# Performance work log

Hardware: AMD Instinct MI355X
Metric: run time of the kernel (lower is better)

The kernel has to match this reference:

```python
import jax, jax.numpy as jnp
import numpy as np

S, C, HF, WF = 6, 64, 44, 80          # cameras, feat channels, feat H, feat W
H_IMG, W_IMG = 352.0, 640.0           # full image size (opt.height/opt.width)
Z, Y, X = 16, 100, 100                # voxel grid (opt.voxels_size)
XMIN, XMAX = -40.0, 40.0
YMIN, YMAX = -40.0, 40.0
ZMIN, ZMAX = -1.0, 5.4
EPS = 1e-6


def setup_inputs() -> dict:
    key = jax.random.key(0)
    features = jax.random.normal(jax.random.fold_in(key, 0), (S, C, HF, WF), dtype=jnp.float32)
    # intrinsics at full image resolution
    K = np.eye(4, dtype=np.float32)
    K[0, 0] = 500.0; K[1, 1] = 500.0
    K[0, 2] = W_IMG / 2.0; K[1, 2] = H_IMG / 2.0
    pix_T_cams = np.tile(K[None], (S, 1, 1))
    # 6-camera surround rig: cam0_T_camX rigid transforms (columns = camera axes in ref frame)
    mats = []
    for i in range(S):
        th = 2.0 * np.pi * i / S
        c, s = np.cos(th), np.sin(th)
        T = np.eye(4, dtype=np.float32)
        T[:3, 0] = [-s, c, 0.0]          # camera x (right)
        T[:3, 1] = [0.0, 0.0, -1.0]      # camera y (down)
        T[:3, 2] = [c, s, 0.0]           # camera z (forward)
        T[:3, 3] = [0.5 * c, 0.5 * s, 1.5]
        mats.append(T)
    cam0_T_camXs = np.stack(mats).astype(np.float32)
    return {"features": features,
            "pix_T_cams": jnp.asarray(pix_T_cams),
            "cam0_T_camXs": jnp.asarray(cam0_T_camXs)}


def _safe_inverse(T):
    # rigid 4x4 inverse: [R t] -> [R^T, -R^T t]
    R = T[:, :3, :3]
    t = T[:, :3, 3]
    Rt = jnp.swapaxes(R, 1, 2)
    tt = -jnp.einsum('sij,sj->si', Rt, t)
    inv = jnp.zeros_like(T)
    inv = inv.at[:, :3, :3].set(Rt).at[:, :3, 3].set(tt).at[:, 3, 3].set(1.0)
    return inv


def _voxel_centers():
    # ref-frame coordinates of voxel centers, flattened [Z*Y*X, 3] with x fastest
    vx = (XMAX - XMIN) / X
    vy = (YMAX - YMIN) / Y
    vz = (ZMAX - ZMIN) / Z
    xs = XMIN + vx * (jnp.arange(X, dtype=jnp.float32) + 0.5)
    ys = YMIN + vy * (jnp.arange(Y, dtype=jnp.float32) + 0.5)
    zs = ZMIN + vz * (jnp.arange(Z, dtype=jnp.float32) + 0.5)
    zz, yy, xx = jnp.meshgrid(zs, ys, xs, indexing='ij')
    return jnp.stack([xx, yy, zz], axis=-1).reshape(-1, 3)


def _bilinear(img, x, y):
    # img: [C,H,W]; x,y: [N] pixel coords; zero padding outside
    Hh, Ww = img.shape[-2], img.shape[-1]
    x0 = jnp.floor(x)
    y0 = jnp.floor(y)
    wx1 = x - x0
    wy1 = y - y0

    def corner(xi, yi, w):
        valid = (xi >= 0) & (xi < Ww) & (yi >= 0) & (yi < Hh)
        xc = jnp.clip(xi, 0, Ww - 1).astype(jnp.int32)
        yc = jnp.clip(yi, 0, Hh - 1).astype(jnp.int32)
        return img[:, yc, xc] * (w * valid)[None, :]

    return (corner(x0, y0, (1 - wx1) * (1 - wy1))
            + corner(x0 + 1, y0, wx1 * (1 - wy1))
            + corner(x0, y0 + 1, (1 - wx1) * wy1)
            + corner(x0 + 1, y0 + 1, wx1 * wy1))  # [C,N]


def reference(features, pix_T_cams, cam0_T_camXs):
    camXs_T_cam0 = _safe_inverse(cam0_T_camXs)
    sx, sy = WF / W_IMG, HF / H_IMG
    scale = jnp.diag(jnp.array([sx, sy, 1.0, 1.0], jnp.float32))
    featpix_T_cams = jnp.einsum('ij,sjk->sik', scale, pix_T_cams)
    pix_T_cam0 = jnp.einsum('sij,sjk->sik', featpix_T_cams, camXs_T_cam0)

    xyz0 = _voxel_centers()                                  # [N,3]
    xyz1 = jnp.concatenate([xyz0, jnp.ones((xyz0.shape[0], 1), jnp.float32)], -1)
    xyz_pix = jnp.einsum('sij,nj->sni', pix_T_cam0, xyz1)    # [S,N,4]
    z_cam = jnp.einsum('sj,nj->sn', camXs_T_cam0[:, 2, :], xyz1)  # camX-frame depth

    denom = jnp.maximum(xyz_pix[..., 2], 1e-6)
    x_pix = xyz_pix[..., 0] / denom
    y_pix = xyz_pix[..., 1] / denom
    valid = ((x_pix > -0.5) & (x_pix < WF - 0.5)
             & (y_pix > -0.5) & (y_pix < HF - 0.5)
             & (z_cam > 0.0))

    # grid_sample(align_corners=False) with norm 2*(p/W)-1 samples at pixel p-0.5
    samp = jax.vmap(_bilinear)(features, x_pix - 0.5, y_pix - 0.5)  # [S,C,N]
    feat_mems = samp * valid[:, None, :].astype(samp.dtype)
    feat_mems = feat_mems.reshape(S, C, Z, Y, X)[None]              # [1,S,C,Z,Y,X]

    mask = (jnp.abs(feat_mems) > 0).astype(feat_mems.dtype)
    feat_mem = (feat_mems * mask).sum(1) / (mask.sum(1) + EPS)      # masked mean over cams
    return jnp.transpose(feat_mem, (0, 1, 4, 3, 2))                 # [1,C,X,Y,Z]
```

## Files before the change

### kernel.cpp

```cpp
#include <hip/hip_runtime.h>

#define NS 6
#define NC 64
#define HF 44
#define WF 80
#define HW (HF * WF)
#define NZ 16
#define NY 100
#define NX 100
#define XYZ (NX * NY * NZ)
#define COLS 4
#define NPAR (COLS * NZ * NS)

typedef float v4f __attribute__((ext_vector_type(4)));

__device__ void compute_mats(int s, const float* __restrict__ pix,
                             const float* __restrict__ c0TX,
                             float* __restrict__ mats) {
    const float* T = c0TX + s * 16;
    float inv[4][4];
    for (int i = 0; i < 3; ++i) {
        for (int j = 0; j < 3; ++j) inv[i][j] = T[j * 4 + i];
        inv[i][3] = -(T[0 * 4 + i] * T[0 * 4 + 3] +
                      T[1 * 4 + i] * T[1 * 4 + 3] +
                      T[2 * 4 + i] * T[2 * 4 + 3]);
    }
    inv[3][0] = 0.f; inv[3][1] = 0.f; inv[3][2] = 0.f; inv[3][3] = 1.f;
    const float sx = (float)WF / 640.0f;
    const float sy = (float)HF / 352.0f;
    const float* K = pix + s * 16;
    float fp[3][4];
    for (int j = 0; j < 4; ++j) {
        fp[0][j] = sx * K[0 * 4 + j];
        fp[1][j] = sy * K[1 * 4 + j];
        fp[2][j] = K[2 * 4 + j];
    }
    float* M = mats + s * 16;
    for (int i = 0; i < 3; ++i)
        for (int j = 0; j < 4; ++j) {
            float acc = 0.f;
            for (int k = 0; k < 4; ++k) acc += fp[i][k] * inv[k][j];
            M[i * 4 + j] = acc;
        }
    for (int j = 0; j < 4; ++j) M[12 + j] = inv[2][j];
}

__global__ __launch_bounds__(256) void transpose_feat(
        const float* __restrict__ in, float* __restrict__ outT,
        const float* __restrict__ pix, const float* __restrict__ c0TX,
        float* __restrict__ mats) {
    __shared__ float tile[64 * 65];
    int b = blockIdx.x;
    int t = threadIdx.x;
    if (b == 0 && t < NS) compute_mats(t, pix, c0TX, mats);
    int s = b / 55;
    int hw0 = (b % 55) * 64;
#pragma unroll
    for (int i = 0; i < 4; ++i) {
        int e = t + i * 256;
        int c = e >> 4, wg = e & 15;
        float4 f = *(const float4*)(in + ((size_t)(s * NC + c)) * HW + hw0 + wg * 4);
        tile[c * 65 + wg * 4 + 0] = f.x;
        tile[c * 65 + wg * 4 + 1] = f.y;
        tile[c * 65 + wg * 4 + 2] = f.z;
        tile[c * 65 + wg * 4 + 3] = f.w;
    }
    __syncthreads();
#pragma unroll
    for (int i = 0; i < 4; ++i) {
        int e = t + i * 256;
        int hwl = e >> 4, cg = e & 15;
        float4 f;
        f.x = tile[(cg * 4 + 0) * 65 + hwl];
        f.y = tile[(cg * 4 + 1) * 65 + hwl];
        f.z = tile[(cg * 4 + 2) * 65 + hwl];
        f.w = tile[(cg * 4 + 3) * 65 + hwl];
        *(float4*)(outT + ((size_t)s * HW + hw0 + hwl) * NC + cg * 4) = f;
    }
}

__global__ void setup_mats(const float* __restrict__ pix,
                           const float* __restrict__ c0TX,
                           float* __restrict__ mats) {
    int s = threadIdx.x;
    if (s < NS) compute_mats(s, pix, c0TX, mats);
}

template <bool TRANS>
__global__ __launch_bounds__(256) void volpool(
        const float* __restrict__ feat,
        const float* __restrict__ mats,
        float* __restrict__ out) {
    __shared__ float4 wts[NPAR];
    __shared__ int4   offs[NPAR];
    __shared__ int    vflags[NPAR];
    __shared__ int    vidx[COLS][NZ][NS];
    __shared__ int    nvalid[COLS][NZ];
    __shared__ float  ostage[COLS][NC * 17];

    int t = threadIdx.x;
    int b = blockIdx.x;
    int x0 = (b % (NX / COLS)) * COLS;
    int y  = b / (NX / COLS);

    for (int p = t; p < NPAR; p += 256) {
        int col  = p / 96;
        int rest = p - col * 96;
        int s = rest % NS;
        int z = rest / NS;
        const float* M = mats + s * 16;
        float xw = -40.0f + 0.8f * ((float)(x0 + col) + 0.5f);
        float yw = -40.0f + 0.8f * ((float)y + 0.5f);
        float zw = -1.0f + 0.4f * ((float)z + 0.5f);
        float px = M[0] * xw + M[1] * yw + M[2]  * zw + M[3];
        float py = M[4] * xw + M[5] * yw + M[6]  * zw + M[7];
        float pz = M[8] * xw + M[9] * yw + M[10] * zw + M[11];
        float zc = M[12] * xw + M[13] * yw + M[14] * zw + M[15];
        float denom = fmaxf(pz, 1e-6f);
        float xp = px / denom, yp = py / denom;
        bool valid = (xp > -0.5f) & (xp < (float)WF - 0.5f) &
                     (yp > -0.5f) & (yp < (float)HF - 0.5f) & (zc > 0.0f);
        vflags[p] = valid ? 1 : 0;
        if (valid) {
            float xs = xp - 0.5f, ys = yp - 0.5f;
            float x0f = floorf(xs), y0f = floorf(ys);
            float wx1 = xs - x0f, wy1 = ys - y0f;
            float wx0 = 1.f - wx1, wy0 = 1.f - wy1;
            int xi0 = (int)x0f, yi0 = (int)y0f;
            int xi1 = xi0 + 1, yi1 = yi0 + 1;
            bool bx0 = (xi0 >= 0) & (xi0 < WF);
            bool bx1 = (xi1 >= 0) & (xi1 < WF);
            bool by0 = (yi0 >= 0) & (yi0 < HF);
            bool by1 = (yi1 >= 0) & (yi1 < HF);
            int x0c = min(max(xi0, 0), WF - 1);
            int x1c = min(max(xi1, 0), WF - 1);
            int y0c = min(max(yi0, 0), HF - 1);
            int y1c = min(max(yi1, 0), HF - 1);
            float4 w;
            w.x = wx0 * wy0 * (float)(bx0 & by0);
            w.y = wx1 * wy0 * (float)(bx1 & by0);
            w.z = wx0 * wy1 * (float)(bx0 & by1);
            w.w = wx1 * wy1 * (float)(bx1 & by1);
            int p00 = y0c * WF + x0c, p10 = y0c * WF + x1c;
            int p01 = y1c * WF + x0c, p11 = y1c * WF + x1c;
            int4 o;
            if (TRANS) {
                o.x = (s * HW + p00) * NC;
                o.y = (s * HW + p10) * NC;
                o.z = (s * HW + p01) * NC;
                o.w = (s * HW + p11) * NC;
            } else {
                o.x = s * NC * HW + p00;
                o.y = s * NC * HW + p10;
                o.z = s * NC * HW + p01;
                o.w = s * NC * HW + p11;
            }
            wts[p] = w;
            offs[p] = o;
        }
    }
    __syncthreads();

    if (t < COLS * NZ) {
        int col = t >> 4, z = t & 15;
        int base = col * 96 + z * NS;
        int n = 0;
        for (int s = 0; s < NS; ++s)
            if (vflags[base + s]) vidx[col][z][n++] = base + s;
        nvalid[col][z] = n;
    }
    __syncthreads();

    int cg = t & 15, z = t >> 4;
    int ch4 = cg << 2;
#pragma unroll
    for (int col = 0; col < COLS; ++col) {
        float4 sum = make_float4(0.f, 0.f, 0.f, 0.f);
        float4 cnt = make_float4(0.f, 0.f, 0.f, 0.f);
        int nv = nvalid[col][z];
        for (int j = 0; j < nv; ++j) {
            int idx = vidx[col][z][j];
            float4 w = wts[idx];
            int4 o = offs[idx];
            float4 f00, f10, f01, f11;
            if (TRANS) {
                f00 = *(const float4*)(feat + o.x + ch4);
                f10 = *(const float4*)(feat + o.y + ch4);
                f01 = *(const float4*)(feat + o.z + ch4);
                f11 = *(const float4*)(feat + o.w + ch4);
            } else {
                f00.x = feat[o.x + (ch4 + 0) * HW]; f00.y = feat[o.x + (ch4 + 1) * HW];
                f00.z = feat[o.x + (ch4 + 2) * HW]; f00.w = feat[o.x + (ch4 + 3) * HW];
                f10.x = feat[o.y + (ch4 + 0) * HW]; f10.y = feat[o.y + (ch4 + 1) * HW];
                f10.z = feat[o.y + (ch4 + 2) * HW]; f10.w = feat[o.y + (ch4 + 3) * HW];
                f01.x = feat[o.z + (ch4 + 0) * HW]; f01.y = feat[o.z + (ch4 + 1) * HW];
                f01.z = feat[o.z + (ch4 + 2) * HW]; f01.w = feat[o.z + (ch4 + 3) * HW];
                f11.x = feat[o.w + (ch4 + 0) * HW]; f11.y = feat[o.w + (ch4 + 1) * HW];
                f11.z = feat[o.w + (ch4 + 2) * HW]; f11.w = feat[o.w + (ch4 + 3) * HW];
            }
            float vx = w.x * f00.x + w.y * f10.x + w.z * f01.x + w.w * f11.x;
            float vy = w.x * f00.y + w.y * f10.y + w.z * f01.y + w.w * f11.y;
            float vz = w.x * f00.z + w.y * f10.z + w.z * f01.z + w.w * f11.z;
            float vw = w.x * f00.w + w.y * f10.w + w.z * f01.w + w.w * f11.w;
            sum.x += vx; cnt.x += (vx != 0.0f) ? 1.0f : 0.0f;
            sum.y += vy; cnt.y += (vy != 0.0f) ? 1.0f : 0.0f;
            sum.z += vz; cnt.z += (vz != 0.0f) ? 1.0f : 0.0f;
            sum.w += vw; cnt.w += (vw != 0.0f) ? 1.0f : 0.0f;
        }
        float* os = &ostage[col][0];
        os[(ch4 + 0) * 17 + z] = sum.x / (cnt.x + 1e-6f);
        os[(ch4 + 1) * 17 + z] = sum.y / (cnt.y + 1e-6f);
        os[(ch4 + 2) * 17 + z] = sum.z / (cnt.z + 1e-6f);
        os[(ch4 + 3) * 17 + z] = sum.w / (cnt.w + 1e-6f);
    }
    __syncthreads();

    int c = t >> 2, zq = t & 3;
#pragma unroll
    for (int col = 0; col < COLS; ++col) {
        v4f v4;
        v4.x = ostage[col][c * 17 + zq * 4 + 0];
        v4.y = ostage[col][c * 17 + zq * 4 + 1];
        v4.z = ostage[col][c * 17 + zq * 4 + 2];
        v4.w = ostage[col][c * 17 + zq * 4 + 3];
        float* o = out + (size_t)c * XYZ +
                   ((size_t)(x0 + col) * NY + y) * NZ + zq * 4;
        __builtin_nontemporal_store(v4, (v4f*)o);
    }
}

extern "C" void kernel_launch(void* const* d_in, const int* in_sizes, int n_in,
                              void* d_out, int out_size, void* d_ws, size_t ws_size,
                              hipStream_t stream) {
    const float* features = (const float*)d_in[0];
    const float* pix      = (const float*)d_in[1];
    const float* c0TX     = (const float*)d_in[2];
    float* out   = (float*)d_out;
    float* mats  = (float*)d_ws;
    float* featT = (float*)((char*)d_ws + 512);
    size_t need = 512 + sizeof(float) * (size_t)NS * HW * NC;

    if (ws_size >= need) {
        hipLaunchKernelGGL(transpose_feat, dim3(NS * 55), dim3(256), 0, stream,
                           features, featT, pix, c0TX, mats);
        hipLaunchKernelGGL((volpool<true>), dim3((NX / COLS) * NY), dim3(256),
                           0, stream, featT, mats, out);
    } else {
        hipLaunchKernelGGL(setup_mats, dim3(1), dim3(64), 0, stream,
                           pix, c0TX, mats);
        hipLaunchKernelGGL((volpool<false>), dim3((NX / COLS) * NY), dim3(256),
                           0, stream, features, mats, out);
    }
}
```

Measured before the change: 89.16 us.

## Process one voxel column per block with compacted samples and software-pipelined gathers

Each block now handles a single (x,y) column instead of four, so the grid has four times as many smaller blocks. Valid camera samples' weights and offsets are compacted into per-z arrays, so the hot loop no longer reads through an index table. The gather loop is software-pipelined so the next camera's loads are issued before the current sample is accumulated. Offsets are precomputed as byte offsets, and the divide by count is replaced by a small reciprocal lookup table. The trade-off is more blocks and more per-block setup and sync overhead, with fewer independent loads in flight per thread.

```diff
diff --git a/kernel.cpp b/kernel.cpp
--- a/kernel.cpp
+++ b/kernel.cpp
@@ -9,8 +9,6 @@
 #define NY 100
 #define NX 100
 #define XYZ (NX * NY * NZ)
-#define COLS 4
-#define NPAR (COLS * NZ * NS)
 
 typedef float v4f __attribute__((ext_vector_type(4)));
 
@@ -91,25 +89,23 @@
         const float* __restrict__ feat,
         const float* __restrict__ mats,
         float* __restrict__ out) {
-    __shared__ float4 wts[NPAR];
-    __shared__ int4   offs[NPAR];
-    __shared__ int    vflags[NPAR];
-    __shared__ int    vidx[COLS][NZ][NS];
-    __shared__ int    nvalid[COLS][NZ];
-    __shared__ float  ostage[COLS][NC * 17];
+    __shared__ float4 wts_raw[96];
+    __shared__ int4   offs_raw[96];
+    __shared__ int    vflags[96];
+    __shared__ float4 wts_c[NZ][NS];
+    __shared__ int4   offs_c[NZ][NS];
+    __shared__ int    nvalid[NZ];
+    __shared__ float  rlut[8];
+    __shared__ float  ostage[NC * 17];
 
     int t = threadIdx.x;
     int b = blockIdx.x;
-    int x0 = (b % (NX / COLS)) * COLS;
-    int y  = b / (NX / COLS);
-
-    for (int p = t; p < NPAR; p += 256) {
-        int col  = p / 96;
-        int rest = p - col * 96;
-        int s = rest % NS;
-        int z = rest / NS;
+    int x = b % NX, y = b / NX;
+
+    if (t < 96) {
+        int s = t % NS, z = t / NS;
         const float* M = mats + s * 16;
-        float xw = -40.0f + 0.8f * ((float)(x0 + col) + 0.5f);
+        float xw = -40.0f + 0.8f * ((float)x + 0.5f);
         float yw = -40.0f + 0.8f * ((float)y + 0.5f);
         float zw = -1.0f + 0.4f * ((float)z + 0.5f);
         float px = M[0] * xw + M[1] * yw + M[2]  * zw + M[3];
@@ -120,7 +116,7 @@
         float xp = px / denom, yp = py / denom;
         bool valid = (xp > -0.5f) & (xp < (float)WF - 0.5f) &
                      (yp > -0.5f) & (yp < (float)HF - 0.5f) & (zc > 0.0f);
-        vflags[p] = valid ? 1 : 0;
+        vflags[t] = valid ? 1 : 0;
         if (valid) {
             float xs = xp - 0.5f, ys = yp - 0.5f;
             float x0f = floorf(xs), y0f = floorf(ys);
@@ -145,88 +141,121 @@
             int p01 = y1c * WF + x0c, p11 = y1c * WF + x1c;
             int4 o;
             if (TRANS) {
-                o.x = (s * HW + p00) * NC;
-                o.y = (s * HW + p10) * NC;
-                o.z = (s * HW + p01) * NC;
-                o.w = (s * HW + p11) * NC;
+                o.x = (s * HW + p00) << 8;
+                o.y = (s * HW + p10) << 8;
+                o.z = (s * HW + p01) << 8;
+                o.w = (s * HW + p11) << 8;
             } else {
-                o.x = s * NC * HW + p00;
-                o.y = s * NC * HW + p10;
-                o.z = s * NC * HW + p01;
-                o.w = s * NC * HW + p11;
+                o.x = (s * NC * HW + p00) << 2;
+                o.y = (s * NC * HW + p10) << 2;
+                o.z = (s * NC * HW + p01) << 2;
+                o.w = (s * NC * HW + p11) << 2;
             }
-            wts[p] = w;
-            offs[p] = o;
-        }
-    }
-    __syncthreads();
-
-    if (t < COLS * NZ) {
-        int col = t >> 4, z = t & 15;
-        int base = col * 96 + z * NS;
+            wts_raw[t] = w;
+            offs_raw[t] = o;
+        }
+    }
+    if (t >= 96 && t < 104) {
+        int k = t - 96;
+        rlut[k] = 1.0f / ((float)k + 1e-6f);
+    }
+    __syncthreads();
+
+    if (t < NZ) {
+        int base = t * NS;
         int n = 0;
-        for (int s = 0; s < NS; ++s)
-            if (vflags[base + s]) vidx[col][z][n++] = base + s;
-        nvalid[col][z] = n;
+        for (int s = 0; s < NS; ++s) {
+            if (vflags[base + s]) {
+                wts_c[t][n] = wts_raw[base + s];
+                offs_c[t][n] = offs_raw[base + s];
+                ++n;
+            }
+        }
+        nvalid[t] = n;
     }
     __syncthreads();
 
     int cg = t & 15, z = t >> 4;
     int ch4 = cg << 2;
-#pragma unroll
-    for (int col = 0; col < COLS; ++col) {
-        float4 sum = make_float4(0.f, 0.f, 0.f, 0.f);
-        float4 cnt = make_float4(0.f, 0.f, 0.f, 0.f);
-        int nv = nvalid[col][z];
-        for (int j = 0; j < nv; ++j) {
-            int idx = vidx[col][z][j];
-            float4 w = wts[idx];
-            int4 o = offs[idx];
-            float4 f00, f10, f01, f11;
+    const char* fb = (const char*)feat + (TRANS ? (cg << 4) : 0);
+    float4 sum = make_float4(0.f, 0.f, 0.f, 0.f);
+    int cx = 0, cy = 0, cz = 0, cw = 0;
+    int nv = nvalid[z];
+    if (nv > 0) {
+        float4 w = wts_c[z][0];
+        int4 o = offs_c[z][0];
+        float4 f00, f10, f01, f11;
+        if (TRANS) {
+            f00 = *(const float4*)(fb + o.x);
+            f10 = *(const float4*)(fb + o.y);
+            f01 = *(const float4*)(fb + o.z);
+            f11 = *(const float4*)(fb + o.w);
+        } else {
+            const float* fp = (const float*)fb;
+            int e00 = o.x >> 2, e10 = o.y >> 2, e01 = o.z >> 2, e11 = o.w >> 2;
+            f00.x = fp[e00 + (ch4+0)*HW]; f00.y = fp[e00 + (ch4+1)*HW];
+            f00.z = fp[e00 + (ch4+2)*HW]; f00.w = fp[e00 + (ch4+3)*HW];
+            f10.x = fp[e10 + (ch4+0)*HW]; f10.y = fp[e10 + (ch4+1)*HW];
+            f10.z = fp[e10 + (ch4+2)*HW]; f10.w = fp[e10 + (ch4+3)*HW];
+            f01.x = fp[e01 + (ch4+0)*HW]; f01.y = fp[e01 + (ch4+1)*HW];
+            f01.z = fp[e01 + (ch4+2)*HW]; f01.w = fp[e01 + (ch4+3)*HW];
+            f11.x = fp[e11 + (ch4+0)*HW]; f11.y = fp[e11 + (ch4+1)*HW];
+            f11.z = fp[e11 + (ch4+2)*HW]; f11.w = fp[e11 + (ch4+3)*HW];
+        }
+        for (int j = 1; j < nv; ++j) {
+            float4 w2 = wts_c[z][j];
+            int4 o2 = offs_c[z][j];
+            float4 g00, g10, g01, g11;
             if (TRANS) {
-                f00 = *(const float4*)(feat + o.x + ch4);
-                f10 = *(const float4*)(feat + o.y + ch4);
-                f01 = *(const float4*)(feat + o.z + ch4);
-                f11 = *(const float4*)(feat + o.w + ch4);
+                g00 = *(const float4*)(fb + o2.x);
+                g10 = *(const float4*)(fb + o2.y);
+                g01 = *(const float4*)(fb + o2.z);
+                g11 = *(const float4*)(fb + o2.w);
             } else {
-                f00.x = feat[o.x + (ch4 + 0) * HW]; f00.y = feat[o.x + (ch4 + 1) * HW];
-                f00.z = feat[o.x + (ch4 + 2) * HW]; f00.w = feat[o.x + (ch4 + 3) * HW];
-                f10.x = feat[o.y + (ch4 + 0) * HW]; f10.y = feat[o.y + (ch4 + 1) * HW];
-                f10.z = feat[o.y + (ch4 + 2) * HW]; f10.w = feat[o.y + (ch4 + 3) * HW];
-                f01.x = feat[o.z + (ch4 + 0) * HW]; f01.y = feat[o.z + (ch4 + 1) * HW];
-                f01.z = feat[o.z + (ch4 + 2) * HW]; f01.w = feat[o.z + (ch4 + 3) * HW];
-                f11.x = feat[o.w + (ch4 + 0) * HW]; f11.y = feat[o.w + (ch4 + 1) * HW];
-                f11.z = feat[o.w + (ch4 + 2) * HW]; f11.w = feat[o.w + (ch4 + 3) * HW];
+                const float* fp = (const float*)fb;
+                int e00 = o2.x >> 2, e10 = o2.y >> 2, e01 = o2.z >> 2, e11 = o2.w >> 2;
+                g00.x = fp[e00 + (ch4+0)*HW]; g00.y = fp[e00 + (ch4+1)*HW];
+                g00.z = fp[e00 + (ch4+2)*HW]; g00.w = fp[e00 + (ch4+3)*HW];
+                g10.x = fp[e10 + (ch4+0)*HW]; g10.y = fp[e10 + (ch4+1)*HW];
+                g10.z = fp[e10 + (ch4+2)*HW]; g10.w = fp[e10 + (ch4+3)*HW];
+                g01.x = fp[e01 + (ch4+0)*HW]; g01.y = fp[e01 + (ch4+1)*HW];
+                g01.z = fp[e01 + (ch4+2)*HW]; g01.w = fp[e01 + (ch4+3)*HW];
+                g11.x = fp[e11 + (ch4+0)*HW]; g11.y = fp[e11 + (ch4+1)*HW];
+                g11.z = fp[e11 + (ch4+2)*HW]; g11.w = fp[e11 + (ch4+3)*HW];
             }
             float vx = w.x * f00.x + w.y * f10.x + w.z * f01.x + w.w * f11.x;
             float vy = w.x * f00.y + w.y * f10.y + w.z * f01.y + w.w * f11.y;
             float vz = w.x * f00.z + w.y * f10.z + w.z * f01.z + w.w * f11.z;
             float vw = w.x * f00.w + w.y * f10.w + w.z * f01.w + w.w * f11.w;
-            sum.x += vx; cnt.x += (vx != 0.0f) ? 1.0f : 0.0f;
-            sum.y += vy; cnt.y += (vy != 0.0f) ? 1.0f : 0.0f;
-            sum.z += vz; cnt.z += (vz != 0.0f) ? 1.0f : 0.0f;
-            sum.w += vw; cnt.w += (vw != 0.0f) ? 1.0f : 0.0f;
-        }
-        float* os = &ostage[col][0];
-        os[(ch4 + 0) * 17 + z] = sum.x / (cnt.x + 1e-6f);
-        os[(ch4 + 1) * 17 + z] = sum.y / (cnt.y + 1e-6f);
-        os[(ch4 + 2) * 17 + z] = sum.z / (cnt.z + 1e-6f);
-        os[(ch4 + 3) * 17 + z] = sum.w / (cnt.w + 1e-6f);
-    }
+            sum.x += vx; cx += (vx != 0.0f);
+            sum.y += vy; cy += (vy != 0.0f);
+            sum.z += vz; cz += (vz != 0.0f);
+            sum.w += vw; cw += (vw != 0.0f);
+            w = w2; f00 = g00; f10 = g10; f01 = g01; f11 = g11;
+        }
+        float vx = w.x * f00.x + w.y * f10.x + w.z * f01.x + w.w * f11.x;
+        float vy = w.x * f00.y + w.y * f10.y + w.z * f01.y + w.w * f11.y;
+        float vz = w.x * f00.z + w.y * f10.z + w.z * f01.z + w.w * f11.z;
+        float vw = w.x * f00.w + w.y * f10.w + w.z * f01.w + w.w * f11.w;
+        sum.x += vx; cx += (vx != 0.0f);
+        sum.y += vy; cy += (vy != 0.0f);
+        sum.z += vz; cz += (vz != 0.0f);
+        sum.w += vw; cw += (vw != 0.0f);
+    }
+    ostage[(ch4 + 0) * 17 + z] = sum.x * rlut[cx];
+    ostage[(ch4 + 1) * 17 + z] = sum.y * rlut[cy];
+    ostage[(ch4 + 2) * 17 + z] = sum.z * rlut[cz];
+    ostage[(ch4 + 3) * 17 + z] = sum.w * rlut[cw];
     __syncthreads();
 
     int c = t >> 2, zq = t & 3;
-#pragma unroll
-    for (int col = 0; col < COLS; ++col) {
-        v4f v4;
-        v4.x = ostage[col][c * 17 + zq * 4 + 0];
-        v4.y = ostage[col][c * 17 + zq * 4 + 1];
-        v4.z = ostage[col][c * 17 + zq * 4 + 2];
-        v4.w = ostage[col][c * 17 + zq * 4 + 3];
-        float* o = out + (size_t)c * XYZ +
-                   ((size_t)(x0 + col) * NY + y) * NZ + zq * 4;
-        __builtin_nontemporal_store(v4, (v4f*)o);
-    }
+    v4f v4;
+    v4.x = ostage[c * 17 + zq * 4 + 0];
+    v4.y = ostage[c * 17 + zq * 4 + 1];
+    v4.z = ostage[c * 17 + zq * 4 + 2];
+    v4.w = ostage[c * 17 + zq * 4 + 3];
+    float* o = out + (size_t)c * XYZ + ((size_t)x * NY + y) * NZ + zq * 4;
+    __builtin_nontemporal_store(v4, (v4f*)o);
 }
 
 extern "C" void kernel_launch(void* const* d_in, const int* in_sizes, int n_in,
@@ -243,12 +272,12 @@
     if (ws_size >= need) {
         hipLaunchKernelGGL(transpose_feat, dim3(NS * 55), dim3(256), 0, stream,
                            features, featT, pix, c0TX, mats);
-        hipLaunchKernelGGL((volpool<true>), dim3((NX / COLS) * NY), dim3(256),
-                           0, stream, featT, mats, out);
+        hipLaunchKernelGGL((volpool<true>), dim3(NX * NY), dim3(256), 0, stream,
+                           featT, mats, out);
     } else {
         hipLaunchKernelGGL(setup_mats, dim3(1), dim3(64), 0, stream,
                            pix, c0TX, mats);
-        hipLaunchKernelGGL((volpool<false>), dim3((NX / COLS) * NY), dim3(256),
-                           0, stream, features, mats, out);
-    }
-}
+        hipLaunchKernelGGL((volpool<false>), dim3(NX * NY), dim3(256), 0, stream,
+                           features, mats, out);
+    }
+}
```

New measurement: 84.61 us. 5.1% less time.
